# Optimization experiments

Measured on AMD Instinct MI355X. Metric: run time of the kernel, lower is better.

Reference implementation:

```python
import jax, jax.numpy as jnp
import numpy as np

B, S, D, H = 2, 2048, 1024, 16
DK = D // H  # 64


def setup_inputs() -> dict:
    key = jax.random.key(0)
    ks = jax.random.split(key, 4)
    scale = 1.0 / np.sqrt(D)
    return {
        "q_input": jax.random.normal(ks[0], (B, S, D), dtype=jnp.float32),
        "W_q": jax.random.normal(ks[1], (D, D), dtype=jnp.float32) * scale,
        "b_q": jnp.zeros((D,), dtype=jnp.float32),
        "W_k": jax.random.normal(ks[2], (D, D), dtype=jnp.float32) * scale,
        "b_k": jnp.zeros((D,), dtype=jnp.float32),
        "W_v": jax.random.normal(ks[3], (D, D), dtype=jnp.float32) * scale,
        "b_v": jnp.zeros((D,), dtype=jnp.float32),
    }


def reference(q_input, W_q, b_q, W_k, b_k, W_v, b_v):
    # Self-attention: k_input and v_input default to q_input in the torch module.
    # nn.Linear computes x @ W.T + b
    q = q_input @ W_q.T + b_q
    k = q_input @ W_k.T + b_k
    v = q_input @ W_v.T + b_v

    # [B,S,D] -> [B,H,S,DK]
    def split_heads(x):
        return x.reshape(B, S, H, DK).transpose(0, 2, 1, 3)

    qh, kh, vh = split_heads(q), split_heads(k), split_heads(v)

    # scores [B,H,S,S]; causal mask added BEFORE scaling (as in source; -inf invariant)
    scores = jnp.einsum("bhqd,bhkd->bhqk", qh, kh)
    causal = jnp.tril(jnp.ones((S, S), dtype=bool))
    scores = jnp.where(causal[None, None], scores, -jnp.inf)
    scores = scores / jnp.sqrt(jnp.float32(DK))
    probs = jax.nn.softmax(scores, axis=-1)
    z = jnp.einsum("bhqk,bhkd->bhqd", probs, vh)  # [B,H,S,DK]
    # [B,H,S,DK] -> [B,S,H,DK] -> [B,S,D]
    return z.transpose(0, 2, 1, 3).reshape(B, S, D)
```

## Files before the change

### kernel.cpp

```cpp
#include <hip/hip_runtime.h>
#include <hip/hip_bf16.h>
#include <stdint.h>

typedef __attribute__((ext_vector_type(8))) short short8;
typedef __attribute__((ext_vector_type(4))) short short4v;
typedef __attribute__((ext_vector_type(4))) float f32x4;
typedef __attribute__((ext_vector_type(16))) float f32x16;

#define B_ 2
#define S_ 2048
#define D_ 1024
#define H_ 16
#define DK_ 64
#define M_ (B_*S_)

#define WS_QKV   0
#define WS_XB    12582912
#define WS_WB    16777216

#define QSCALE (0.125f * 1.44269504088896f)

#define GLL16(g, l) __builtin_amdgcn_global_load_lds( \
    (const __attribute__((address_space(1))) void*)(g), \
    (__attribute__((address_space(3))) void*)(l), 16, 0, 0)

#define WAIT_VM0 asm volatile("s_waitcnt vmcnt(0)" ::: "memory")
#define WAIT_VM4 asm volatile("s_waitcnt vmcnt(4)" ::: "memory")
#define WAIT_VM8 asm volatile("s_waitcnt vmcnt(8)" ::: "memory")
#define WAIT_LGKM0 asm volatile("s_waitcnt lgkmcnt(0)" ::: "memory")
#define BARRIER_RAW asm volatile("s_barrier" ::: "memory")

static __device__ __forceinline__ short f2bf(float f){
  union { float f; unsigned u; } x; x.f = f;
  unsigned r = x.u + 0x7fff + ((x.u >> 16) & 1);
  return (short)(r >> 16);
}

__global__ __launch_bounds__(256) void cvt_bf16(
    const float* __restrict__ X,  const float* __restrict__ Wq,
    const float* __restrict__ Wk, const float* __restrict__ Wv,
    short* __restrict__ ws)
{
  const int z = blockIdx.z;
  const float* src; short* dst; int n;
  if (z == 0)      { src = X;  dst = ws + WS_XB;               n = M_*D_; }
  else if (z == 1) { src = Wq; dst = ws + WS_WB;               n = D_*D_; }
  else if (z == 2) { src = Wk; dst = ws + WS_WB + D_*D_;       n = D_*D_; }
  else             { src = Wv; dst = ws + WS_WB + 2*(D_*D_);   n = D_*D_; }
  const int stride = gridDim.x * blockDim.x * 4;
  for (int i = (blockIdx.x * blockDim.x + threadIdx.x) * 4; i < n; i += stride) {
    float4 v = *(const float4*)(src + i);
    short4v o;
    o.x = f2bf(v.x); o.y = f2bf(v.y); o.z = f2bf(v.z); o.w = f2bf(v.w);
    *(short4v*)(dst + i) = o;
  }
}

__global__ __launch_bounds__(512, 2) void qkv_gemm(
    const short* __restrict__ ws_in,
    const float* __restrict__ bq, const float* __restrict__ bk,
    const float* __restrict__ bv, short* __restrict__ qkv)
{
  const int z = blockIdx.z;
  const short* X  = ws_in + WS_XB;
  const short* Wm = ws_in + WS_WB + (size_t)z * (D_*D_);
  short* out = qkv + (size_t)z * (M_*D_);

  __shared__ __align__(16) short lds[65536];

  const int t = threadIdx.x;
  const int w = t >> 6, lane = t & 63;
  const int quad = lane >> 4, l16 = lane & 15;
  const int wm = w >> 2, wn = w & 3;
  const int m0 = blockIdx.y * 256, n0 = blockIdx.x * 256;

  const int rl = t >> 2;
  const int sl = (t & 3) ^ (rl & 3);
  const short* sA0 = X  + (size_t)(m0 + rl) * D_ + sl*8;
  const short* sA1 = sA0 + (size_t)128 * D_;
  const short* sB0 = Wm + (size_t)(n0 + rl) * D_ + sl*8;
  const short* sB1 = sB0 + (size_t)128 * D_;
  const int ldsw = w << 9;

  const int swz = quad ^ (l16 & 3);

  f32x4 acc[8][4];
  #pragma unroll
  for (int i=0;i<8;i++)
    #pragma unroll
    for (int j=0;j<4;j++) acc[i][j] = (f32x4){0.f,0.f,0.f,0.f};

  #pragma unroll
  for (int p=0;p<3;p++){
    GLL16(sA0 + p*32, lds + p*16384 + ldsw);
    GLL16(sA1 + p*32, lds + p*16384 + 4096 + ldsw);
    GLL16(sB0 + p*32, lds + p*16384 + 8192 + ldsw);
    GLL16(sB1 + p*32, lds + p*16384 + 12288 + ldsw);
  }
  WAIT_VM8;
  BARRIER_RAW;

  for (int kt = 0; kt < 32; kt++) {
    const int bf = kt & 3;
    const short* bufA = lds + bf*16384;
    const short* bufB = bufA + 8192;
    const int tb = (kt + 3) & 3;
    const int ko2 = (kt + 3) * 32;
    const bool st = (kt + 3) < 32;

    short8 aF[4], bF[4];
    #pragma unroll
    for (int mf=0; mf<4; mf++)
      aF[mf] = *(const short8*)(bufA + (wm*128 + mf*16 + l16)*32 + swz*8);
    #pragma unroll
    for (int nf=0; nf<4; nf++)
      bF[nf] = *(const short8*)(bufB + (wn*64 + nf*16 + l16)*32 + swz*8);
    if (st) {
      GLL16(sA0 + ko2, lds + tb*16384 + ldsw);
      GLL16(sA1 + ko2, lds + tb*16384 + 4096 + ldsw);
    }
    BARRIER_RAW;
    WAIT_LGKM0;
    __builtin_amdgcn_s_setprio(1);
    #pragma unroll
    for (int mf=0; mf<4; mf++)
      #pragma unroll
      for (int nf=0; nf<4; nf++)
        acc[mf][nf] = __builtin_amdgcn_mfma_f32_16x16x32_bf16(aF[mf], bF[nf], acc[mf][nf], 0,0,0);
    __builtin_amdgcn_s_setprio(0);
    BARRIER_RAW;

    #pragma unroll
    for (int mf=0; mf<4; mf++)
      aF[mf] = *(const short8*)(bufA + (wm*128 + 64 + mf*16 + l16)*32 + swz*8);
    if (st) {
      GLL16(sB0 + ko2, lds + tb*16384 + 8192 + ldsw);
      GLL16(sB1 + ko2, lds + tb*16384 + 12288 + ldsw);
    }
    BARRIER_RAW;
    WAIT_LGKM0;
    __builtin_amdgcn_s_setprio(1);
    #pragma unroll
    for (int mf=0; mf<4; mf++)
      #pragma unroll
      for (int nf=0; nf<4; nf++)
        acc[4+mf][nf] = __builtin_amdgcn_mfma_f32_16x16x32_bf16(aF[mf], bF[nf], acc[4+mf][nf], 0,0,0);
    __builtin_amdgcn_s_setprio(0);
    if      (kt < 29)  { WAIT_VM8; }
    else if (kt == 29) { WAIT_VM4; }
    else if (kt == 30) { WAIT_VM0; }
    BARRIER_RAW;
  }

  __syncthreads();

  if (z != 2) {
    const float scale = (z==0) ? QSCALE : 1.0f;
    const float* bias = (z==0) ? bq : bk;
    float bv4[4];
    #pragma unroll
    for (int nf=0; nf<4; nf++) bv4[nf] = bias[n0 + wn*64 + nf*16 + l16];
    short* ep = lds;
    #pragma unroll
    for (int p=0; p<2; p++){
      if (wm == p){
        #pragma unroll
        for (int mf=0; mf<8; mf++)
          #pragma unroll
          for (int nf=0; nf<4; nf++)
            #pragma unroll
            for (int i=0; i<4; i++)
              ep[(mf*16 + quad*4 + i)*264 + wn*64 + nf*16 + l16] =
                  f2bf((acc[mf][nf][i] + bv4[nf]) * scale);
      }
      __syncthreads();
      #pragma unroll
      for (int it=0; it<8; it++){
        const int cid = it*512 + t;
        const int row = cid >> 5, cc = cid & 31;
        short8 vv = *(const short8*)(ep + row*264 + cc*8);
        const int m = m0 + p*128 + row, bidx = m >> 11, s = m & 2047;
        const int n = n0 + cc*8, h = n >> 6, dd = n & 63;
        *(short8*)(out + (((size_t)(bidx*H_ + h))*S_ + s)*DK_ + dd) = vv;
      }
      __syncthreads();
    }
  } else {
    float bv4[4];
    #pragma unroll
    for (int nf=0; nf<4; nf++) bv4[nf] = bv[n0 + wn*64 + nf*16 + l16];
    short* ep = lds;
    #pragma unroll
    for (int p=0; p<2; p++){
      if (wm == p){
        #pragma unroll
        for (int mf=0; mf<8; mf++)
          #pragma unroll
          for (int nf=0; nf<4; nf++)
            #pragma unroll
            for (int i=0; i<4; i++)
              ep[(wn*64 + nf*16 + l16)*136 + mf*16 + quad*4 + i] =
                  f2bf(acc[mf][nf][i] + bv4[nf]);
      }
      __syncthreads();
      #pragma unroll
      for (int it=0; it<8; it++){
        const int cid = it*512 + t;
        const int row = cid >> 4, cc = cid & 15;
        short8 vv = *(const short8*)(ep + row*136 + cc*8);
        const int n = n0 + row, h = n >> 6, dd = n & 63;
        const int m0p = m0 + p*128;
        const int bidx = m0p >> 11;
        const int s = (m0p & 2047) + cc*8;
        *(short8*)(out + (((size_t)(bidx*H_ + h))*DK_ + dd)*S_ + s) = vv;
      }
      __syncthreads();
    }
  }
}

__global__ __launch_bounds__(256, 1) void attn(
    const short* __restrict__ qkv, float* __restrict__ out)
{
  const int id = blockIdx.x;
  const int slot = id >> 3;
  const int bh = (id & 7) + 8*(slot & 3);
  const int p  = slot >> 2;
  const int nA = 2*p + 2;

  const short* Q  = qkv + (size_t)bh * (S_*DK_);
  const short* K  = Q + (size_t)(M_*D_);
  const short* VT = qkv + (size_t)(2*M_*D_) + (size_t)bh * (DK_*S_);

  __shared__ short Kbuf[3][4096];
  __shared__ short Vbuf[3][4096];

  const int t = threadIdx.x;
  const int w = t >> 6, lane = t & 63;
  const int l32 = lane & 31, h = lane >> 5;
  const int xrow = l32 & 7;

  const int qA0 = p*128 + w*32;
  const int qB0 = (15-p)*128 + w*32;

  short8 bqA[4], bqB[4];
  #pragma unroll
  for (int dc=0; dc<4; dc++){
    bqA[dc] = *(const short8*)(Q + (size_t)(qA0 + l32)*DK_ + dc*16 + h*8);
    bqB[dc] = *(const short8*)(Q + (size_t)(qB0 + l32)*DK_ + dc*16 + h*8);
  }
  #pragma unroll
  for (int dc=0; dc<4; dc++){
    asm volatile("" : "+v"(bqA[dc]));
    asm volatile("" : "+v"(bqB[dc]));
  }

  const int r8   = lane >> 3;
  const int sc8  = ((lane & 7) ^ r8) * 8;
  const int row0 = w*16 + r8;

  #pragma unroll
  for (int pt=0; pt<3; pt++){
    const int kb = (pt < nA ? pt : pt - nA) * 64;
    #pragma unroll
    for (int j=0; j<2; j++){
      GLL16(K  + (size_t)(kb + row0 + j*8)*DK_ + sc8, &Kbuf[pt][0] + w*1024 + j*512);
      GLL16(VT + (size_t)(row0 + j*8)*S_ + kb + sc8,  &Vbuf[pt][0] + w*1024 + j*512);
    }
  }
  WAIT_VM8;
  BARRIER_RAW;

  f32x16 o0 = {0.f,0.f,0.f,0.f,0.f,0.f,0.f,0.f,0.f,0.f,0.f,0.f,0.f,0.f,0.f,0.f};
  f32x16 o1 = o0;
  float lsum = 0.f;
  const int bb = bh >> 4, hh = bh & 15;

  int cur = 0;
  for (int ft = 0; ft < 34; ft++){
    const bool segB = ft >= nA;
    const int kb   = (segB ? ft - nA : ft) * 64;
    const int q0w  = segB ? qB0 : qA0;
    const bool active = (kb <= q0w + 31);
    const short* Kc = &Kbuf[cur][0];
    const short* Vc = &Vbuf[cur][0];

    short8 ak[8], vk[8];
    if (active){
      #pragma unroll
      for (int dc=0; dc<4; dc++){
        const int xk = ((dc*2 + h) ^ xrow)*8;
        ak[dc]   = *(const short8*)(Kc + l32*64 + xk);
        ak[4+dc] = *(const short8*)(Kc + (32 + l32)*64 + xk);
        vk[dc]   = *(const short8*)(Vc + l32*64 + xk);
        vk[4+dc] = *(const short8*)(Vc + (32 + l32)*64 + xk);
      }
    }
    WAIT_LGKM0;
    BARRIER_RAW;

    if (ft + 3 < 34){
      const int f3 = ft + 3;
      const int kbp = (f3 < nA ? f3 : f3 - nA) * 64;
      #pragma unroll
      for (int j=0; j<2; j++){
        GLL16(K  + (size_t)(kbp + row0 + j*8)*DK_ + sc8, &Kbuf[cur][0] + w*1024 + j*512);
        GLL16(VT + (size_t)(row0 + j*8)*S_ + kbp + sc8,  &Vbuf[cur][0] + w*1024 + j*512);
      }
    }

    if (active){
      f32x16 s[2];
      s[0] = o0 - o0;
      s[1] = s[0];
      #pragma unroll
      for (int dc=0; dc<4; dc++){
        const short8 bqv = segB ? bqB[dc] : bqA[dc];
        s[0] = __builtin_amdgcn_mfma_f32_32x32x16_bf16(ak[dc],   bqv, s[0], 0,0,0);
        s[1] = __builtin_amdgcn_mfma_f32_32x32x16_bf16(ak[4+dc], bqv, s[1], 0,0,0);
      }

      if (kb + 63 > q0w) {
        const int qg = q0w + l32;
        #pragma unroll
        for (int r=0; r<16; r++){
          const int k0 = kb + (r&3) + 8*(r>>2) + 4*h;
          if (k0      > qg) s[0][r] = -3.0e38f;
          if (k0 + 32 > qg) s[1][r] = -3.0e38f;
        }
      }

      short8 pf[4];
      #pragma unroll
      for (int mk=0; mk<2; mk++){
        #pragma unroll
        for (int u=0; u<2; u++){
          float p0 = __builtin_amdgcn_exp2f(s[mk][8*u+0]);
          float p1 = __builtin_amdgcn_exp2f(s[mk][8*u+1]);
          float p2 = __builtin_amdgcn_exp2f(s[mk][8*u+2]);
          float p3 = __builtin_amdgcn_exp2f(s[mk][8*u+3]);
          float p4 = __builtin_amdgcn_exp2f(s[mk][8*u+4]);
          float p5 = __builtin_amdgcn_exp2f(s[mk][8*u+5]);
          float p6 = __builtin_amdgcn_exp2f(s[mk][8*u+6]);
          float p7 = __builtin_amdgcn_exp2f(s[mk][8*u+7]);
          lsum += ((p0+p1)+(p2+p3)) + ((p4+p5)+(p6+p7));
          unsigned X0, X1, Y0, Y1;
          asm("v_cvt_pk_bf16_f32 %0, %1, %2" : "=v"(X0) : "v"(p0), "v"(p1));
          asm("v_cvt_pk_bf16_f32 %0, %1, %2" : "=v"(X1) : "v"(p2), "v"(p3));
          asm("v_cvt_pk_bf16_f32 %0, %1, %2" : "=v"(Y0) : "v"(p4), "v"(p5));
          asm("v_cvt_pk_bf16_f32 %0, %1, %2" : "=v"(Y1) : "v"(p6), "v"(p7));
          asm("v_permlane32_swap_b32 %0, %1" : "+v"(X0), "+v"(Y0));
          asm("v_permlane32_swap_b32 %0, %1" : "+v"(X1), "+v"(Y1));
          union { unsigned u4[4]; short8 s8; } pp;
          pp.u4[0] = X0; pp.u4[1] = X1; pp.u4[2] = Y0; pp.u4[3] = Y1;
          pf[mk*2 + u] = pp.s8;
        }
      }

      #pragma unroll
      for (int kk=0; kk<4; kk++){
        o0 = __builtin_amdgcn_mfma_f32_32x32x16_bf16(pf[kk], vk[kk],   o0, 0,0,0);
        o1 = __builtin_amdgcn_mfma_f32_32x32x16_bf16(pf[kk], vk[4+kk], o1, 0,0,0);
      }
    }

    if (ft == nA - 1){
      float rs = lsum + __shfl_xor(lsum, 32, 64);
      float linv = 1.0f / rs;
      #pragma unroll
      for (int r=0; r<16; r++){
        const int qrow = (r&3) + 8*(r>>2) + 4*h;
        const float lw = __shfl(linv, qrow, 64);
        float* dst = out + ((size_t)bb*S_ + (qA0 + qrow))*D_ + hh*DK_;
        dst[l32]      = o0[r] * lw;
        dst[32 + l32] = o1[r] * lw;
      }
      o0 = o0 - o0; o1 = o1 - o1; lsum = 0.f;
    }

    {
      const int rem = 33 - ft;
      if      (rem >= 3) { WAIT_VM8; }
      else if (rem == 2) { WAIT_VM4; }
      else if (rem == 1) { WAIT_VM0; }
    }
    BARRIER_RAW;
    cur = (cur == 2) ? 0 : cur + 1;
  }

  {
    float rs = lsum + __shfl_xor(lsum, 32, 64);
    float linv = 1.0f / rs;
    #pragma unroll
    for (int r=0; r<16; r++){
      const int qrow = (r&3) + 8*(r>>2) + 4*h;
      const float lw = __shfl(linv, qrow, 64);
      float* dst = out + ((size_t)bb*S_ + (qB0 + qrow))*D_ + hh*DK_;
      dst[l32]      = o0[r] * lw;
      dst[32 + l32] = o1[r] * lw;
    }
  }
}

extern "C" void kernel_launch(void* const* d_in, const int* in_sizes, int n_in,
                              void* d_out, int out_size, void* d_ws, size_t ws_size,
                              hipStream_t stream)
{
  (void)in_sizes; (void)n_in; (void)out_size; (void)ws_size;
  const float* X  = (const float*)d_in[0];
  const float* Wq = (const float*)d_in[1];
  const float* bq = (const float*)d_in[2];
  const float* Wk = (const float*)d_in[3];
  const float* bk = (const float*)d_in[4];
  const float* Wv = (const float*)d_in[5];
  const float* bv = (const float*)d_in[6];
  short* ws  = (short*)d_ws;
  float* out = (float*)d_out;

  dim3 g0(1024, 1, 4);
  cvt_bf16<<<g0, dim3(256,1,1), 0, stream>>>(X, Wq, Wk, Wv, ws);
  dim3 g1(D_/256, M_/256, 3);
  qkv_gemm<<<g1, dim3(512,1,1), 0, stream>>>(ws, bq, bk, bv, ws + WS_QKV);
  dim3 g2(256, 1);
  attn<<<g2, dim3(256,1,1), 0, stream>>>(ws + WS_QKV, out);
}
```

Before: 177.2 us.

## Use four-stage LDS ring to drop mid-iteration barrier and split attention segments

The K/V LDS ring grows from three to four slots, so the prefetch for tile ft+3 writes a slot that no wave is still reading. This removes the per-iteration lgkm wait and the barrier that sat between the LDS reads and the async loads, leaving one barrier per tile. The loop is also split into two segment calls, which removes the per-iteration segB selects and the in-loop output store branch. The cost is more LDS per block and some code duplication from inlining the segment body twice.

```diff
diff --git a/kernel.cpp b/kernel.cpp
--- a/kernel.cpp
+++ b/kernel.cpp
@@ -219,74 +219,35 @@
   }
 }
 
-__global__ __launch_bounds__(256, 1) void attn(
-    const short* __restrict__ qkv, float* __restrict__ out)
-{
-  const int id = blockIdx.x;
-  const int slot = id >> 3;
-  const int bh = (id & 7) + 8*(slot & 3);
-  const int p  = slot >> 2;
-  const int nA = 2*p + 2;
-
-  const short* Q  = qkv + (size_t)bh * (S_*DK_);
-  const short* K  = Q + (size_t)(M_*D_);
-  const short* VT = qkv + (size_t)(2*M_*D_) + (size_t)bh * (DK_*S_);
-
-  __shared__ short Kbuf[3][4096];
-  __shared__ short Vbuf[3][4096];
-
-  const int t = threadIdx.x;
-  const int w = t >> 6, lane = t & 63;
-  const int l32 = lane & 31, h = lane >> 5;
-  const int xrow = l32 & 7;
-
-  const int qA0 = p*128 + w*32;
-  const int qB0 = (15-p)*128 + w*32;
-
-  short8 bqA[4], bqB[4];
-  #pragma unroll
-  for (int dc=0; dc<4; dc++){
-    bqA[dc] = *(const short8*)(Q + (size_t)(qA0 + l32)*DK_ + dc*16 + h*8);
-    bqB[dc] = *(const short8*)(Q + (size_t)(qB0 + l32)*DK_ + dc*16 + h*8);
-  }
-  #pragma unroll
-  for (int dc=0; dc<4; dc++){
-    asm volatile("" : "+v"(bqA[dc]));
-    asm volatile("" : "+v"(bqB[dc]));
-  }
-
-  const int r8   = lane >> 3;
-  const int sc8  = ((lane & 7) ^ r8) * 8;
-  const int row0 = w*16 + r8;
-
-  #pragma unroll
-  for (int pt=0; pt<3; pt++){
-    const int kb = (pt < nA ? pt : pt - nA) * 64;
-    #pragma unroll
-    for (int j=0; j<2; j++){
-      GLL16(K  + (size_t)(kb + row0 + j*8)*DK_ + sc8, &Kbuf[pt][0] + w*1024 + j*512);
-      GLL16(VT + (size_t)(row0 + j*8)*S_ + kb + sc8,  &Vbuf[pt][0] + w*1024 + j*512);
-    }
-  }
-  WAIT_VM8;
-  BARRIER_RAW;
-
-  f32x16 o0 = {0.f,0.f,0.f,0.f,0.f,0.f,0.f,0.f,0.f,0.f,0.f,0.f,0.f,0.f,0.f,0.f};
-  f32x16 o1 = o0;
-  float lsum = 0.f;
-  const int bb = bh >> 4, hh = bh & 15;
-
-  int cur = 0;
-  for (int ft = 0; ft < 34; ft++){
-    const bool segB = ft >= nA;
-    const int kb   = (segB ? ft - nA : ft) * 64;
-    const int q0w  = segB ? qB0 : qA0;
-    const bool active = (kb <= q0w + 31);
-    const short* Kc = &Kbuf[cur][0];
-    const short* Vc = &Vbuf[cur][0];
-
-    short8 ak[8], vk[8];
-    if (active){
+static __device__ __forceinline__ void attn_seg(
+    const int n, const int nA, const int q0w, const short8* __restrict__ bqv,
+    const short* __restrict__ K, const short* __restrict__ VT,
+    short (*Kbuf)[4096], short (*Vbuf)[4096],
+    int& ftg, const int w, const int l32, const int h, const int xrow,
+    const int row0, const int sc8,
+    f32x16& o0, f32x16& o1, float& lsum)
+{
+  for (int it = 0; it < n; ++it, ++ftg){
+    const int cur = ftg & 3;
+
+    if (ftg + 3 < 34){
+      const int f3 = ftg + 3;
+      const int kbp = (f3 < nA ? f3 : f3 - nA) * 64;
+      short* Kn = &Kbuf[f3 & 3][0];
+      short* Vn = &Vbuf[f3 & 3][0];
+      #pragma unroll
+      for (int j=0; j<2; j++){
+        GLL16(K  + (size_t)(kbp + row0 + j*8)*DK_ + sc8, Kn + w*1024 + j*512);
+        GLL16(VT + (size_t)(row0 + j*8)*S_ + kbp + sc8,  Vn + w*1024 + j*512);
+      }
+    }
+
+    const int kb = it*64;
+    if (kb <= q0w + 31){
+      const short* Kc = &Kbuf[cur][0];
+      const short* Vc = &Vbuf[cur][0];
+
+      short8 ak[8], vk[8];
       #pragma unroll
       for (int dc=0; dc<4; dc++){
         const int xk = ((dc*2 + h) ^ xrow)*8;
@@ -295,29 +256,14 @@
         vk[dc]   = *(const short8*)(Vc + l32*64 + xk);
         vk[4+dc] = *(const short8*)(Vc + (32 + l32)*64 + xk);
       }
-    }
-    WAIT_LGKM0;
-    BARRIER_RAW;
-
-    if (ft + 3 < 34){
-      const int f3 = ft + 3;
-      const int kbp = (f3 < nA ? f3 : f3 - nA) * 64;
-      #pragma unroll
-      for (int j=0; j<2; j++){
-        GLL16(K  + (size_t)(kbp + row0 + j*8)*DK_ + sc8, &Kbuf[cur][0] + w*1024 + j*512);
-        GLL16(VT + (size_t)(row0 + j*8)*S_ + kbp + sc8,  &Vbuf[cur][0] + w*1024 + j*512);
-      }
-    }
-
-    if (active){
+
       f32x16 s[2];
       s[0] = o0 - o0;
       s[1] = s[0];
       #pragma unroll
       for (int dc=0; dc<4; dc++){
-        const short8 bqv = segB ? bqB[dc] : bqA[dc];
-        s[0] = __builtin_amdgcn_mfma_f32_32x32x16_bf16(ak[dc],   bqv, s[0], 0,0,0);
-        s[1] = __builtin_amdgcn_mfma_f32_32x32x16_bf16(ak[4+dc], bqv, s[1], 0,0,0);
+        s[0] = __builtin_amdgcn_mfma_f32_32x32x16_bf16(ak[dc],   bqv[dc], s[0], 0,0,0);
+        s[1] = __builtin_amdgcn_mfma_f32_32x32x16_bf16(ak[4+dc], bqv[dc], s[1], 0,0,0);
       }
 
       if (kb + 63 > q0w) {
@@ -364,42 +310,97 @@
       }
     }
 
-    if (ft == nA - 1){
-      float rs = lsum + __shfl_xor(lsum, 32, 64);
-      float linv = 1.0f / rs;
-      #pragma unroll
-      for (int r=0; r<16; r++){
-        const int qrow = (r&3) + 8*(r>>2) + 4*h;
-        const float lw = __shfl(linv, qrow, 64);
-        float* dst = out + ((size_t)bb*S_ + (qA0 + qrow))*D_ + hh*DK_;
-        dst[l32]      = o0[r] * lw;
-        dst[32 + l32] = o1[r] * lw;
-      }
-      o0 = o0 - o0; o1 = o1 - o1; lsum = 0.f;
-    }
-
-    {
-      const int rem = 33 - ft;
-      if      (rem >= 3) { WAIT_VM8; }
-      else if (rem == 2) { WAIT_VM4; }
-      else if (rem == 1) { WAIT_VM0; }
-    }
-    BARRIER_RAW;
-    cur = (cur == 2) ? 0 : cur + 1;
-  }
-
-  {
-    float rs = lsum + __shfl_xor(lsum, 32, 64);
-    float linv = 1.0f / rs;
-    #pragma unroll
-    for (int r=0; r<16; r++){
-      const int qrow = (r&3) + 8*(r>>2) + 4*h;
-      const float lw = __shfl(linv, qrow, 64);
-      float* dst = out + ((size_t)bb*S_ + (qB0 + qrow))*D_ + hh*DK_;
-      dst[l32]      = o0[r] * lw;
-      dst[32 + l32] = o1[r] * lw;
-    }
-  }
+    const int rem = 33 - ftg;
+    if      (rem >= 3) { WAIT_VM8; }
+    else if (rem == 2) { WAIT_VM4; }
+    else if (rem == 1) { WAIT_VM0; }
+    if (ftg < 33) BARRIER_RAW;
+  }
+}
+
+static __device__ __forceinline__ void attn_store(
+    float* __restrict__ out, const int bb, const int hh, const int q0,
+    const int h, const int l32, const f32x16& o0, const f32x16& o1,
+    const float lsum)
+{
+  float rs = lsum + __shfl_xor(lsum, 32, 64);
+  float linv = 1.0f / rs;
+  #pragma unroll
+  for (int r=0; r<16; r++){
+    const int qrow = (r&3) + 8*(r>>2) + 4*h;
+    const float lw = __shfl(linv, qrow, 64);
+    float* dst = out + ((size_t)bb*S_ + (q0 + qrow))*D_ + hh*DK_;
+    dst[l32]      = o0[r] * lw;
+    dst[32 + l32] = o1[r] * lw;
+  }
+}
+
+__global__ __launch_bounds__(256, 1) void attn(
+    const short* __restrict__ qkv, float* __restrict__ out)
+{
+  const int id = blockIdx.x;
+  const int slot = id >> 3;
+  const int bh = (id & 7) + 8*(slot & 3);
+  const int p  = slot >> 2;
+  const int nA = 2*p + 2;
+
+  const short* Q  = qkv + (size_t)bh * (S_*DK_);
+  const short* K  = Q + (size_t)(M_*D_);
+  const short* VT = qkv + (size_t)(2*M_*D_) + (size_t)bh * (DK_*S_);
+
+  __shared__ short Kbuf[4][4096];
+  __shared__ short Vbuf[4][4096];
+
+  const int t = threadIdx.x;
+  const int w = t >> 6, lane = t & 63;
+  const int l32 = lane & 31, h = lane >> 5;
+  const int xrow = l32 & 7;
+
+  const int qA0 = p*128 + w*32;
+  const int qB0 = (15-p)*128 + w*32;
+
+  short8 bqA[4], bqB[4];
+  #pragma unroll
+  for (int dc=0; dc<4; dc++){
+    bqA[dc] = *(const short8*)(Q + (size_t)(qA0 + l32)*DK_ + dc*16 + h*8);
+    bqB[dc] = *(const short8*)(Q + (size_t)(qB0 + l32)*DK_ + dc*16 + h*8);
+  }
+  #pragma unroll
+  for (int dc=0; dc<4; dc++){
+    asm volatile("" : "+v"(bqA[dc]));
+    asm volatile("" : "+v"(bqB[dc]));
+  }
+
+  const int r8   = lane >> 3;
+  const int sc8  = ((lane & 7) ^ r8) * 8;
+  const int row0 = w*16 + r8;
+
+  #pragma unroll
+  for (int pt=0; pt<3; pt++){
+    const int kb = (pt < nA ? pt : pt - nA) * 64;
+    #pragma unroll
+    for (int j=0; j<2; j++){
+      GLL16(K  + (size_t)(kb + row0 + j*8)*DK_ + sc8, &Kbuf[pt][0] + w*1024 + j*512);
+      GLL16(VT + (size_t)(row0 + j*8)*S_ + kb + sc8,  &Vbuf[pt][0] + w*1024 + j*512);
+    }
+  }
+  WAIT_VM8;
+  BARRIER_RAW;
+
+  f32x16 o0 = {0.f,0.f,0.f,0.f,0.f,0.f,0.f,0.f,0.f,0.f,0.f,0.f,0.f,0.f,0.f,0.f};
+  f32x16 o1 = o0;
+  float lsum = 0.f;
+  const int bb = bh >> 4, hh = bh & 15;
+
+  int ftg = 0;
+  attn_seg(nA, nA, qA0, bqA, K, VT, Kbuf, Vbuf,
+           ftg, w, l32, h, xrow, row0, sc8, o0, o1, lsum);
+  attn_store(out, bb, hh, qA0, h, l32, o0, o1, lsum);
+  o0 = o0 - o0; o1 = o1 - o1; lsum = 0.f;
+
+  attn_seg(34 - nA, nA, qB0, bqB, K, VT, Kbuf, Vbuf,
+           ftg, w, l32, h, xrow, row0, sc8, o0, o1, lsum);
+  attn_store(out, bb, hh, qB0, h, l32, o0, o1, lsum);
 }
 
 extern "C" void kernel_launch(void* const* d_in, const int* in_sizes, int n_in,
```

Result: no change. 177.5 us (+0.2%).

## Split attention key tiles across two wave groups and merge partial outputs via LDS

Applied to the files above, without the earlier changes.

The attention kernel moves from 256 to 512 threads per block. Two groups of four waves each process alternating 64-key tiles for the same query rows. Each group accumulates its own output and row sum, and the two are added through a shared-memory merge before normalisation and store. K/V staging uses a 4-slot ring, with each tile loaded by all 8 waves. The aim is more waves in flight per CU to hide latency on a grid of only 256 blocks, at the cost of extra LDS, a merge barrier, and a more intricate step/barrier schedule.

```diff
diff --git a/kernel.cpp b/kernel.cpp
--- a/kernel.cpp
+++ b/kernel.cpp
@@ -219,71 +219,22 @@
   }
 }
 
-__global__ __launch_bounds__(256, 1) void attn(
-    const short* __restrict__ qkv, float* __restrict__ out)
-{
-  const int id = blockIdx.x;
-  const int slot = id >> 3;
-  const int bh = (id & 7) + 8*(slot & 3);
-  const int p  = slot >> 2;
-  const int nA = 2*p + 2;
-
-  const short* Q  = qkv + (size_t)bh * (S_*DK_);
-  const short* K  = Q + (size_t)(M_*D_);
-  const short* VT = qkv + (size_t)(2*M_*D_) + (size_t)bh * (DK_*S_);
-
-  __shared__ short Kbuf[3][4096];
-  __shared__ short Vbuf[3][4096];
-
-  const int t = threadIdx.x;
-  const int w = t >> 6, lane = t & 63;
-  const int l32 = lane & 31, h = lane >> 5;
-  const int xrow = l32 & 7;
-
-  const int qA0 = p*128 + w*32;
-  const int qB0 = (15-p)*128 + w*32;
-
-  short8 bqA[4], bqB[4];
-  #pragma unroll
-  for (int dc=0; dc<4; dc++){
-    bqA[dc] = *(const short8*)(Q + (size_t)(qA0 + l32)*DK_ + dc*16 + h*8);
-    bqB[dc] = *(const short8*)(Q + (size_t)(qB0 + l32)*DK_ + dc*16 + h*8);
-  }
-  #pragma unroll
-  for (int dc=0; dc<4; dc++){
-    asm volatile("" : "+v"(bqA[dc]));
-    asm volatile("" : "+v"(bqB[dc]));
-  }
-
-  const int r8   = lane >> 3;
-  const int sc8  = ((lane & 7) ^ r8) * 8;
-  const int row0 = w*16 + r8;
-
-  #pragma unroll
-  for (int pt=0; pt<3; pt++){
-    const int kb = (pt < nA ? pt : pt - nA) * 64;
-    #pragma unroll
-    for (int j=0; j<2; j++){
-      GLL16(K  + (size_t)(kb + row0 + j*8)*DK_ + sc8, &Kbuf[pt][0] + w*1024 + j*512);
-      GLL16(VT + (size_t)(row0 + j*8)*S_ + kb + sc8,  &Vbuf[pt][0] + w*1024 + j*512);
-    }
-  }
-  WAIT_VM8;
-  BARRIER_RAW;
-
-  f32x16 o0 = {0.f,0.f,0.f,0.f,0.f,0.f,0.f,0.f,0.f,0.f,0.f,0.f,0.f,0.f,0.f,0.f};
-  f32x16 o1 = o0;
-  float lsum = 0.f;
-  const int bb = bh >> 4, hh = bh & 15;
-
-  int cur = 0;
-  for (int ft = 0; ft < 34; ft++){
-    const bool segB = ft >= nA;
-    const int kb   = (segB ? ft - nA : ft) * 64;
-    const int q0w  = segB ? qB0 : qA0;
+static __device__ __forceinline__ void attn_steps(
+    const int nSteps, const int I0, const int nA, const int q0w,
+    const short8* __restrict__ bqv,
+    const short* __restrict__ K, const short* __restrict__ VT,
+    short (*Kbuf)[4096], short (*Vbuf)[4096],
+    const int g, const int w, const int l32, const int h, const int xrow,
+    const int row0, const int sc8,
+    f32x16& o0, f32x16& o1, float& lsum)
+{
+  for (int j = 0; j < nSteps; ++j){
+    const int I  = I0 + j;
+    const int gt = 2*I + g;
+    const int kb = (2*j + g)*64;
     const bool active = (kb <= q0w + 31);
-    const short* Kc = &Kbuf[cur][0];
-    const short* Vc = &Vbuf[cur][0];
+    const short* Kc = &Kbuf[gt & 3][0];
+    const short* Vc = &Vbuf[gt & 3][0];
 
     short8 ak[8], vk[8];
     if (active){
@@ -299,25 +250,24 @@
     WAIT_LGKM0;
     BARRIER_RAW;
 
-    if (ft + 3 < 34){
-      const int f3 = ft + 3;
-      const int kbp = (f3 < nA ? f3 : f3 - nA) * 64;
-      #pragma unroll
-      for (int j=0; j<2; j++){
-        GLL16(K  + (size_t)(kbp + row0 + j*8)*DK_ + sc8, &Kbuf[cur][0] + w*1024 + j*512);
-        GLL16(VT + (size_t)(row0 + j*8)*S_ + kbp + sc8,  &Vbuf[cur][0] + w*1024 + j*512);
+    #pragma unroll
+    for (int q=0; q<2; q++){
+      const int gp = 2*I + 4 + q;
+      if (gp < 34){
+        const int kbp = (gp < nA ? gp : gp - nA) * 64;
+        GLL16(K  + (size_t)(kbp + row0)*DK_ + sc8, &Kbuf[gp & 3][0] + w*512);
+        GLL16(VT + (size_t)row0*S_ + kbp + sc8,    &Vbuf[gp & 3][0] + w*512);
       }
     }
 
     if (active){
       f32x16 s[2];
-      s[0] = o0 - o0;
-      s[1] = s[0];
+      #pragma unroll
+      for (int e=0;e<16;e++){ s[0][e] = 0.f; s[1][e] = 0.f; }
       #pragma unroll
       for (int dc=0; dc<4; dc++){
-        const short8 bqv = segB ? bqB[dc] : bqA[dc];
-        s[0] = __builtin_amdgcn_mfma_f32_32x32x16_bf16(ak[dc],   bqv, s[0], 0,0,0);
-        s[1] = __builtin_amdgcn_mfma_f32_32x32x16_bf16(ak[4+dc], bqv, s[1], 0,0,0);
+        s[0] = __builtin_amdgcn_mfma_f32_32x32x16_bf16(ak[dc],   bqv[dc], s[0], 0,0,0);
+        s[1] = __builtin_amdgcn_mfma_f32_32x32x16_bf16(ak[4+dc], bqv[dc], s[1], 0,0,0);
       }
 
       if (kb + 63 > q0w) {
@@ -364,42 +314,115 @@
       }
     }
 
-    if (ft == nA - 1){
-      float rs = lsum + __shfl_xor(lsum, 32, 64);
-      float linv = 1.0f / rs;
-      #pragma unroll
-      for (int r=0; r<16; r++){
-        const int qrow = (r&3) + 8*(r>>2) + 4*h;
-        const float lw = __shfl(linv, qrow, 64);
-        float* dst = out + ((size_t)bb*S_ + (qA0 + qrow))*D_ + hh*DK_;
-        dst[l32]      = o0[r] * lw;
-        dst[32 + l32] = o1[r] * lw;
-      }
-      o0 = o0 - o0; o1 = o1 - o1; lsum = 0.f;
-    }
-
-    {
-      const int rem = 33 - ft;
-      if      (rem >= 3) { WAIT_VM8; }
-      else if (rem == 2) { WAIT_VM4; }
-      else if (rem == 1) { WAIT_VM0; }
-    }
-    BARRIER_RAW;
-    cur = (cur == 2) ? 0 : cur + 1;
-  }
-
-  {
-    float rs = lsum + __shfl_xor(lsum, 32, 64);
+    if      (I < 15)  { WAIT_VM4; }
+    else if (I == 15) { WAIT_VM0; }
+    if (I < 16) BARRIER_RAW;
+  }
+}
+
+static __device__ __forceinline__ void attn_merge_store(
+    float* __restrict__ out, const int bb, const int hh, const int qbase,
+    const int w, const int wq, const int lane, const int l32, const int h,
+    f32x16& o0, f32x16& o1, float& lsum,
+    float (*ms)[64][33])
+{
+  if (w >= 4){
+    #pragma unroll
+    for (int e=0; e<16; e++){
+      ms[wq][lane][e]    = o0[e];
+      ms[wq][lane][16+e] = o1[e];
+    }
+    ms[wq][lane][32] = lsum;
+  }
+  WAIT_LGKM0;
+  BARRIER_RAW;
+  if (w < 4){
+    #pragma unroll
+    for (int e=0; e<16; e++){
+      o0[e] += ms[wq][lane][e];
+      o1[e] += ms[wq][lane][16+e];
+    }
+    float ls = lsum + ms[wq][lane][32];
+    float rs = ls + __shfl_xor(ls, 32, 64);
     float linv = 1.0f / rs;
     #pragma unroll
     for (int r=0; r<16; r++){
       const int qrow = (r&3) + 8*(r>>2) + 4*h;
       const float lw = __shfl(linv, qrow, 64);
-      float* dst = out + ((size_t)bb*S_ + (qB0 + qrow))*D_ + hh*DK_;
+      float* dst = out + ((size_t)bb*S_ + (qbase + qrow))*D_ + hh*DK_;
       dst[l32]      = o0[r] * lw;
       dst[32 + l32] = o1[r] * lw;
     }
   }
+  #pragma unroll
+  for (int e=0; e<16; e++){ o0[e] = 0.f; o1[e] = 0.f; }
+  lsum = 0.f;
+}
+
+__global__ __launch_bounds__(512, 1) void attn(
+    const short* __restrict__ qkv, float* __restrict__ out)
+{
+  const int id = blockIdx.x;
+  const int slot = id >> 3;
+  const int bh = (id & 7) + 8*(slot & 3);
+  const int p  = slot >> 2;
+  const int nA = 2*p + 2;
+
+  const short* Q  = qkv + (size_t)bh * (S_*DK_);
+  const short* K  = Q + (size_t)(M_*D_);
+  const short* VT = qkv + (size_t)(2*M_*D_) + (size_t)bh * (DK_*S_);
+
+  __shared__ short Kbuf[4][4096];
+  __shared__ short Vbuf[4][4096];
+  __shared__ float ms[4][64][33];
+
+  const int t = threadIdx.x;
+  const int w = t >> 6, lane = t & 63;
+  const int g = w >> 2, wq = w & 3;
+  const int l32 = lane & 31, h = lane >> 5;
+  const int xrow = l32 & 7;
+
+  const int qA0 = p*128 + wq*32;
+  const int qB0 = (15-p)*128 + wq*32;
+
+  short8 bqA[4], bqB[4];
+  #pragma unroll
+  for (int dc=0; dc<4; dc++){
+    bqA[dc] = *(const short8*)(Q + (size_t)(qA0 + l32)*DK_ + dc*16 + h*8);
+    bqB[dc] = *(const short8*)(Q + (size_t)(qB0 + l32)*DK_ + dc*16 + h*8);
+  }
+  #pragma unroll
+  for (int dc=0; dc<4; dc++){
+    asm volatile("" : "+v"(bqA[dc]));
+    asm volatile("" : "+v"(bqB[dc]));
+  }
+
+  const int r8   = lane >> 3;
+  const int sc8  = ((lane & 7) ^ r8) * 8;
+  const int row0 = w*8 + r8;
+
+  #pragma unroll
+  for (int pt=0; pt<4; pt++){
+    const int kb = (pt < nA ? pt : pt - nA) * 64;
+    GLL16(K  + (size_t)(kb + row0)*DK_ + sc8, &Kbuf[pt][0] + w*512);
+    GLL16(VT + (size_t)row0*S_ + kb + sc8,    &Vbuf[pt][0] + w*512);
+  }
+  WAIT_VM4;
+  BARRIER_RAW;
+
+  f32x16 o0, o1;
+  #pragma unroll
+  for (int e=0; e<16; e++){ o0[e] = 0.f; o1[e] = 0.f; }
+  float lsum = 0.f;
+  const int bb = bh >> 4, hh = bh & 15;
+
+  attn_steps(nA/2, 0, nA, qA0, bqA, K, VT, Kbuf, Vbuf,
+             g, w, l32, h, xrow, row0, sc8, o0, o1, lsum);
+  attn_merge_store(out, bb, hh, qA0, w, wq, lane, l32, h, o0, o1, lsum, ms);
+
+  attn_steps(17 - nA/2, nA/2, nA, qB0, bqB, K, VT, Kbuf, Vbuf,
+             g, w, l32, h, xrow, row0, sc8, o0, o1, lsum);
+  attn_merge_store(out, bb, hh, qB0, w, wq, lane, l32, h, o0, o1, lsum, ms);
 }
 
 extern "C" void kernel_launch(void* const* d_in, const int* in_sizes, int n_in,
@@ -422,5 +445,5 @@
   dim3 g1(D_/256, M_/256, 3);
   qkv_gemm<<<g1, dim3(512,1,1), 0, stream>>>(ws, bq, bk, bv, ws + WS_QKV);
   dim3 g2(256, 1);
-  attn<<<g2, dim3(256,1,1), 0, stream>>>(ws + WS_QKV, out);
-}
+  attn<<<g2, dim3(512,1,1), 0, stream>>>(ws + WS_QKV, out);
+}
```

Result: faster. 161.2 us (-9.0%).
